# Kernel optimization log

Hardware: AMD Instinct MI355X
Metric: run time of the kernel (lower is better)

The kernel has to match this reference:

```python
import jax, jax.numpy as jnp
import numpy as np

DIM = 256
HEADS = 8
CAMS = 6
MINSIZE = 25  # AdaptiveAvgPool2d output size = min(feature_map_size)


def layernorm(x, g, b, eps=1e-5):
    mu = x.mean(-1, keepdims=True)
    var = ((x - mu) ** 2).mean(-1, keepdims=True)
    return (x - mu) / jnp.sqrt(var + eps) * g + b


def setup_inputs() -> dict:
    key = jax.random.key(0)
    ks = jax.random.split(key, 16)
    d, n = DIM, CAMS
    s = 0.02
    inp = {}
    inp["q"] = jax.random.normal(ks[0], (2, n, d, 50, 50), jnp.float32)
    inp["k"] = jax.random.normal(ks[1], (2, n, d, 50, 50), jnp.float32)
    inp["v"] = jax.random.normal(ks[2], (2, n, d, 50, 50), jnp.float32)
    inp["Wq"] = jax.random.normal(ks[3], (d, d), jnp.float32) * s
    inp["bq"] = jnp.zeros((d,), jnp.float32)
    inp["Wk"] = jax.random.normal(ks[4], (d, d), jnp.float32) * s
    inp["bk"] = jnp.zeros((d,), jnp.float32)
    inp["Wv"] = jax.random.normal(ks[5], (d, d), jnp.float32) * s
    inp["bv"] = jnp.zeros((d,), jnp.float32)
    inp["Wproj"] = jax.random.normal(ks[6], (n * d, d), jnp.float32) * s
    inp["bproj"] = jnp.zeros((d,), jnp.float32)
    inp["Waddq"] = jax.random.normal(ks[7], (n * d, d), jnp.float32) * s
    inp["baddq"] = jnp.zeros((d,), jnp.float32)
    inp["W1"] = jax.random.normal(ks[8], (d, 2 * d), jnp.float32) * s
    inp["b1"] = jnp.zeros((2 * d,), jnp.float32)
    inp["W2"] = jax.random.normal(ks[9], (2 * d, d), jnp.float32) * s
    inp["b2"] = jnp.zeros((d,), jnp.float32)
    inp["g_pre"] = jnp.ones((n * d,), jnp.float32)
    inp["b_pre"] = jnp.zeros((n * d,), jnp.float32)
    inp["g_norm"] = jnp.ones((d,), jnp.float32)
    inp["b_norm"] = jnp.zeros((d,), jnp.float32)
    return inp


def reference(q, k, v, Wq, bq, Wk, bk, Wv, bv, Wproj, bproj, Waddq, baddq,
              W1, b1, W2, b2, g_pre, b_pre, g_norm, b_norm):
    B, n, d, H, W = q.shape
    m = HEADS
    dh = d // m
    Q = H * W

    # residual query path: (b n d H W) -> (b HW (n d)) -> add_qproj -> (b HW d)
    add_q = jnp.transpose(q, (0, 3, 4, 1, 2)).reshape(B, Q, n * d) @ Waddq + baddq

    # queries: (b n d H W) -> (b n HW d) -> to_q
    qf = jnp.transpose(q, (0, 1, 3, 4, 2)).reshape(B, n, Q, d) @ Wq + bq

    # adaptive avg pool to MINSIZE (exact 2x2 bins since 50 = 2*25)
    def pool(t):
        _, _, _, h, w = t.shape
        return t.reshape(B, n, d, MINSIZE, h // MINSIZE, MINSIZE, w // MINSIZE).mean((4, 6))

    kp = pool(k)  # (b n d 25 25)
    vp = pool(v)
    K = MINSIZE * MINSIZE
    # (avg pool commutes with the pointwise linear to_k/to_v)
    kf = jnp.transpose(kp, (0, 1, 3, 4, 2)).reshape(B, n, K, d) @ Wk + bk
    vf = jnp.transpose(vp, (0, 1, 3, 4, 2)).reshape(B, n, K, d) @ Wv + bv

    # split heads
    qh = qf.reshape(B, n, Q, m, dh)
    kh = kf.reshape(B, n, K, m, dh)
    vh = vf.reshape(B, n, K, m, dh)

    # per-camera scores, softmax jointly over concatenated camera keys
    scores = (dh ** -0.5) * jnp.einsum('bnqmd,bnkmd->bmqnk', qh, kh)  # (B,m,Q,n,K)
    attn = jax.nn.softmax(scores.reshape(B, m, Q, n * K), axis=-1).reshape(B, m, Q, n, K)

    # per-camera attention output, concat cams (and heads within each cam) -> (B,Q,n*d)
    out = jnp.einsum('bmqnk,bnkmd->bqnmd', attn, vh).reshape(B, Q, n * d)

    x = layernorm(out, g_pre, b_pre) @ Wproj + bproj  # (B,Q,d)
    x = x + add_q
    h1 = jax.nn.gelu(x @ W1 + b1, approximate=False)
    x = x + layernorm(h1 @ W2 + b2, g_norm, b_norm)
    return jnp.transpose(x.reshape(B, H, W, d), (0, 3, 1, 2))  # (B,d,H,W)
```

## Files before the change

kernel.cpp:

```cpp
#include <hip/hip_runtime.h>
#include <math.h>

#define BATCH 2
#define NCAM 6
#define DIM 256
#define HEADS 8
#define DH 32
#define HW 2500
#define KP 625
#define NDIM (NCAM*DIM)

typedef __attribute__((ext_vector_type(8))) short short8;
typedef __attribute__((ext_vector_type(4))) float f32x4;

__device__ __forceinline__ short f2bf(float f) {
    union { float f; unsigned u; } v; v.f = f;
    unsigned r = v.u + 0x7fffu + ((v.u >> 16) & 1u);
    return (short)(r >> 16);
}
__device__ __forceinline__ float bf2f(short h) {
    union { unsigned u; float f; } v; v.u = ((unsigned)(unsigned short)h) << 16;
    return v.f;
}

struct WJ { const float* src; short* dst; int K, N; };
struct WArgs { WJ j[7]; };

__global__ __launch_bounds__(256) void prep_all(
    const float* __restrict__ q, const float* __restrict__ k,
    const float* __restrict__ v, short* __restrict__ qbf,
    short* __restrict__ kpbf, short* __restrict__ vpbf, WArgs wa)
{
    __shared__ float t[32][33];
    const int tx = threadIdx.x & 31, ty = threadIdx.x >> 5;
    int i = blockIdx.x;
    if (i < 7584) {
        int slab = i / 632, rem = i % 632;
        int hwB = (rem % 79) * 32, dB = (rem / 79) * 32;
        const float* src = q + (size_t)slab * 640000;
#pragma unroll
        for (int ii = 0; ii < 32; ii += 8) {
            int hw = hwB + tx;
            t[ty + ii][tx] = (hw < HW) ? src[(size_t)(dB + ty + ii) * HW + hw] : 0.f;
        }
        __syncthreads();
#pragma unroll
        for (int ii = 0; ii < 32; ii += 8) {
            int hw = hwB + ty + ii;
            if (hw < HW)
                qbf[((size_t)slab * HW + hw) * DIM + dB + tx] = f2bf(t[tx][ty + ii]);
        }
    } else if (i < 11424) {
        int i2 = i - 7584;
        const float* base; short* dst;
        if (i2 < 1920) { base = k; dst = kpbf; }
        else           { base = v; dst = vpbf; i2 -= 1920; }
        int slab = i2 / 160, rem = i2 % 160;
        int kpB = (rem % 20) * 32, dB = (rem / 20) * 32;
        const float* src = base + (size_t)slab * 640000;
        dst += (size_t)slab * (KP * DIM);
#pragma unroll
        for (int ii = 0; ii < 32; ii += 8) {
            int kp = kpB + tx;
            float val = 0.f;
            if (kp < KP) {
                int r2 = (kp / 25) * 2, c2 = (kp % 25) * 2;
                const float* p0 = src + (size_t)(dB + ty + ii) * HW + r2 * 50 + c2;
                val = 0.25f * (p0[0] + p0[1] + p0[50] + p0[51]);
            }
            t[ty + ii][tx] = val;
        }
        __syncthreads();
#pragma unroll
        for (int ii = 0; ii < 32; ii += 8) {
            int kp = kpB + ty + ii;
            if (kp < KP)
                dst[(size_t)kp * DIM + dB + tx] = f2bf(t[tx][ty + ii]);
        }
    } else {
        int wi = i - 11424;
        WJ jb = wa.j[0];
        for (int jj = 0; jj < 7; jj++) {
            jb = wa.j[jj];
            int cnt = (jb.K >> 5) * (jb.N >> 5);
            if (wi < cnt) break;
            wi -= cnt;
        }
        int tn = jb.N >> 5;
        int nB = (wi % tn) * 32, kB = (wi / tn) * 32;
#pragma unroll
        for (int ii = 0; ii < 32; ii += 8)
            t[ty + ii][tx] = jb.src[(size_t)(kB + ty + ii) * jb.N + nB + tx];
        __syncthreads();
#pragma unroll
        for (int ii = 0; ii < 32; ii += 8)
            jb.dst[(size_t)(nB + ty + ii) * jb.K + kB + tx] = f2bf(t[tx][ty + ii]);
    }
}

struct GJob { const short* A; const short* Bt; const float* bias;
              short* Cb; float* Cf; int M, K, yb, mode; };
struct GArgs { GJob j[4]; };

__global__ __launch_bounds__(256) void gemm_in(GArgs ga) {
    GJob jb = ga.j[blockIdx.z];
    if ((int)blockIdx.y >= jb.yb) return;
    __shared__ short As[128 * 32];
    __shared__ short Bs[64 * 32];

    const int tid  = threadIdx.x;
    const int nB   = blockIdx.x * 64;
    const int rB   = blockIdx.y * 128;
    const int w    = tid >> 6;
    const int lane = tid & 63;
    const int l15  = lane & 15;
    const int quad = lane >> 4;
    const int M = jb.M, K = jb.K;

    f32x4 acc[2][4];
#pragma unroll
    for (int i = 0; i < 2; i++)
#pragma unroll
        for (int jt = 0; jt < 4; jt++) acc[i][jt] = (f32x4){0.f, 0.f, 0.f, 0.f};

    const int ra = tid >> 1, k0 = (tid & 1) * 16;
    const int rga = rB + ra;
    const int bb = rga / 2500, hwp = rga % 2500;
    const int nb_ = tid >> 2, gkb = tid & 3;

    short8 pa0 = {0,0,0,0,0,0,0,0}, pa1 = pa0, pb = pa0;
    if (rga < M) {
        if (jb.mode) {
            int cam = k0 >> 8, c = k0 & 255;
            const short* p = &jb.A[(((size_t)(bb * 6 + cam)) * HW + hwp) * DIM + c];
            pa0 = *(const short8*)p; pa1 = *(const short8*)(p + 8);
        } else {
            const short* p = &jb.A[(size_t)rga * K + k0];
            pa0 = *(const short8*)p; pa1 = *(const short8*)(p + 8);
        }
    }
    pb = *(const short8*)&jb.Bt[(size_t)(nB + nb_) * K + gkb * 8];

    for (int kB = 0; kB < K; kB += 32) {
        __syncthreads();
        {
            int g0 = k0 >> 3;
            *(short8*)&As[ra * 32 + ((g0 ^ (ra & 3)) << 3)]       = pa0;
            *(short8*)&As[ra * 32 + (((g0 + 1) ^ (ra & 3)) << 3)] = pa1;
            *(short8*)&Bs[nb_ * 32 + ((gkb ^ (nb_ & 3)) << 3)]    = pb;
        }
        __syncthreads();
        int kN = kB + 32;
        if (kN < K) {
            if (rga < M) {
                if (jb.mode) {
                    int kk = kN + k0;
                    int cam = kk >> 8, c = kk & 255;
                    const short* p = &jb.A[(((size_t)(bb * 6 + cam)) * HW + hwp) * DIM + c];
                    pa0 = *(const short8*)p; pa1 = *(const short8*)(p + 8);
                } else {
                    const short* p = &jb.A[(size_t)rga * K + kN + k0];
                    pa0 = *(const short8*)p; pa1 = *(const short8*)(p + 8);
                }
            }
            pb = *(const short8*)&jb.Bt[(size_t)(nB + nb_) * K + kN + gkb * 8];
        }
        short8 af[2], bfr[4];
#pragma unroll
        for (int i = 0; i < 2; i++) {
            int m = w * 32 + i * 16 + l15;
            af[i] = *(const short8*)&As[m * 32 + ((quad ^ (m & 3)) << 3)];
        }
#pragma unroll
        for (int jt = 0; jt < 4; jt++) {
            int n = jt * 16 + l15;
            bfr[jt] = *(const short8*)&Bs[n * 32 + ((quad ^ (n & 3)) << 3)];
        }
#pragma unroll
        for (int i = 0; i < 2; i++)
#pragma unroll
            for (int jt = 0; jt < 4; jt++)
                acc[i][jt] = __builtin_amdgcn_mfma_f32_16x16x32_bf16(
                    af[i], bfr[jt], acc[i][jt], 0, 0, 0);
    }
#pragma unroll
    for (int i = 0; i < 2; i++) {
        int rbase = rB + w * 32 + i * 16 + quad * 4;
#pragma unroll
        for (int jt = 0; jt < 4; jt++) {
            int col = nB + jt * 16 + l15;
            float bcol = jb.bias[col];
#pragma unroll
            for (int reg = 0; reg < 4; reg++) {
                int rr = rbase + reg;
                if (rr < M) {
                    float vv = acc[i][jt][reg] + bcol;
                    if (jb.Cb) jb.Cb[(size_t)rr * 256 + col] = f2bf(vv);
                    else       jb.Cf[(size_t)rr * 256 + col] = vv;
                }
            }
        }
    }
}

template<int EPI, int WF32, int WBF>
__global__ __launch_bounds__(256) void mgemm_bf(
    const short* __restrict__ A, const short* __restrict__ Bt,
    const float* __restrict__ bias, const float* __restrict__ res,
    float* __restrict__ C, short* __restrict__ C2, int M, int N, int K)
{
    __shared__ short As[128 * 32];
    __shared__ short Bs[64 * 32];

    const int tid  = threadIdx.x;
    const int nB   = blockIdx.x * 64;
    const int rB   = blockIdx.y * 128;
    const int w    = tid >> 6;
    const int lane = tid & 63;
    const int l15  = lane & 15;
    const int quad = lane >> 4;

    f32x4 acc[2][4];
#pragma unroll
    for (int i = 0; i < 2; i++)
#pragma unroll
        for (int jt = 0; jt < 4; jt++) acc[i][jt] = (f32x4){0.f, 0.f, 0.f, 0.f};

    const int ra = tid >> 1, k0 = (tid & 1) * 16;
    const int rga = rB + ra;
    const int nb_ = tid >> 2, gkb = tid & 3;

    short8 pa0 = {0,0,0,0,0,0,0,0}, pa1 = pa0, pb = pa0;
    if (rga < M) {
        const short* p = &A[(size_t)rga * K + k0];
        pa0 = *(const short8*)p; pa1 = *(const short8*)(p + 8);
    }
    pb = *(const short8*)&Bt[(size_t)(nB + nb_) * K + gkb * 8];

    for (int kB = 0; kB < K; kB += 32) {
        __syncthreads();
        {
            int g0 = k0 >> 3;
            *(short8*)&As[ra * 32 + ((g0 ^ (ra & 3)) << 3)]       = pa0;
            *(short8*)&As[ra * 32 + (((g0 + 1) ^ (ra & 3)) << 3)] = pa1;
            *(short8*)&Bs[nb_ * 32 + ((gkb ^ (nb_ & 3)) << 3)]    = pb;
        }
        __syncthreads();
        int kN = kB + 32;
        if (kN < K) {
            if (rga < M) {
                const short* p = &A[(size_t)rga * K + kN + k0];
                pa0 = *(const short8*)p; pa1 = *(const short8*)(p + 8);
            }
            pb = *(const short8*)&Bt[(size_t)(nB + nb_) * K + kN + gkb * 8];
        }
        short8 af[2], bfr[4];
#pragma unroll
        for (int i = 0; i < 2; i++) {
            int m = w * 32 + i * 16 + l15;
            af[i] = *(const short8*)&As[m * 32 + ((quad ^ (m & 3)) << 3)];
        }
#pragma unroll
        for (int jt = 0; jt < 4; jt++) {
            int n = jt * 16 + l15;
            bfr[jt] = *(const short8*)&Bs[n * 32 + ((quad ^ (n & 3)) << 3)];
        }
#pragma unroll
        for (int i = 0; i < 2; i++)
#pragma unroll
            for (int jt = 0; jt < 4; jt++)
                acc[i][jt] = __builtin_amdgcn_mfma_f32_16x16x32_bf16(
                    af[i], bfr[jt], acc[i][jt], 0, 0, 0);
    }
#pragma unroll
    for (int i = 0; i < 2; i++) {
        int rbase = rB + w * 32 + i * 16 + quad * 4;
#pragma unroll
        for (int jt = 0; jt < 4; jt++) {
            int col = nB + jt * 16 + l15;
            float bcol = bias[col];
#pragma unroll
            for (int reg = 0; reg < 4; reg++) {
                int rr = rbase + reg;
                if (rr < M) {
                    float vv = acc[i][jt][reg] + bcol;
                    if (EPI == 1) vv = 0.5f * vv * (1.f + erff(vv * 0.70710678118654752f));
                    if (EPI == 2) vv += res[(size_t)rr * N + col];
                    if (WF32) C[(size_t)rr * N + col] = vv;
                    if (WBF)  C2[(size_t)rr * N + col] = f2bf(vv);
                }
            }
        }
    }
}

#define TQA 64
#define CH 64
#define VSTR 72

__global__ __launch_bounds__(256) void attn_mfma(
    const short* __restrict__ qf, const short* __restrict__ kf,
    const short* __restrict__ vf, short* __restrict__ attn_out,
    float* __restrict__ Zp)
{
    const int qt  = blockIdx.x;
    const int bm  = blockIdx.y;
    const int cam = blockIdx.z;
    const int b = bm >> 3, m = bm & 7;
    const int q0 = qt * TQA;
    const int tid = threadIdx.x;
    const int w = tid >> 6, lane = tid & 63;
    const int l15 = lane & 15, quad = lane >> 4;

    __shared__ __align__(16) short Ks[CH][DH];
    __shared__ __align__(16) short Vt[DH][VSTR];
    __shared__ __align__(16) short Pl[TQA][VSTR];

    const size_t slab = (size_t)(b * 6 + cam);

    int qrow = q0 + w * 16 + l15;
    int qcl  = qrow < HW ? qrow : HW - 1;
    const short8 aq = *(const short8*)&qf[(slab * HW + qcl) * DIM + m * DH + quad * 8];

    const short* kb = kf + slab * KP * DIM + m * DH;
    const short* vb = vf + slab * KP * DIM + m * DH;

    f32x4 oacc[2];
    oacc[0] = (f32x4){0.f, 0.f, 0.f, 0.f};
    oacc[1] = (f32x4){0.f, 0.f, 0.f, 0.f};
    float zp[4] = {0.f, 0.f, 0.f, 0.f};
    const float scale = 0.17677669529663687f;

    const int kl = tid >> 2, d8 = (tid & 3) * 8;
    const int vcol = (((kl >> 3) ^ (d8 >> 3)) << 3) | (kl & 7);

    for (int c0 = 0; c0 < KP; c0 += CH) {
        __syncthreads();
        {
            int key = c0 + kl;
            short8 kv8 = {0, 0, 0, 0, 0, 0, 0, 0};
            short8 vv8 = {0, 0, 0, 0, 0, 0, 0, 0};
            if (key < KP) {
                kv8 = *(const short8*)&kb[(size_t)key * DIM + d8];
                vv8 = *(const short8*)&vb[(size_t)key * DIM + d8];
            }
            *(short8*)&Ks[kl][d8] = kv8;
#pragma unroll
            for (int t = 0; t < 8; t++) Vt[d8 + t][vcol] = vv8[t];
        }
        __syncthreads();
        f32x4 sfrag[4];
#pragma unroll
        for (int jt = 0; jt < 4; jt++) {
            short8 bk8 = *(const short8*)&Ks[jt * 16 + l15][quad * 8];
            sfrag[jt] = __builtin_amdgcn_mfma_f32_16x16x32_bf16(
                aq, bk8, (f32x4){0.f, 0.f, 0.f, 0.f}, 0, 0, 0);
        }
#pragma unroll
        for (int jt = 0; jt < 4; jt++) {
            bool valid = (c0 + jt * 16 + l15) < KP;
#pragma unroll
            for (int reg = 0; reg < 4; reg++) {
                float p = valid ? __expf(scale * sfrag[jt][reg]) : 0.f;
                short ph = f2bf(p);
                zp[reg] += bf2f(ph);
                Pl[w * 16 + quad * 4 + reg][jt * 16 + l15] = ph;
            }
        }
#pragma unroll
        for (int ks = 0; ks < 2; ks++) {
            short8 ap = *(const short8*)&Pl[w * 16 + l15][ks * 32 + quad * 8];
#pragma unroll
            for (int nt = 0; nt < 2; nt++) {
                int dhn = nt * 16 + l15;
                int pgrp = ((ks * 4 + quad) ^ (dhn >> 3));
                short8 bv8 = *(const short8*)&Vt[dhn][pgrp << 3];
                oacc[nt] = __builtin_amdgcn_mfma_f32_16x16x32_bf16(
                    ap, bv8, oacc[nt], 0, 0, 0);
            }
        }
    }
#pragma unroll
    for (int off = 1; off < 16; off <<= 1)
#pragma unroll
        for (int reg = 0; reg < 4; reg++)
            zp[reg] += __shfl_xor(zp[reg], off, 64);
#pragma unroll
    for (int reg = 0; reg < 4; reg++) {
        int q = q0 + w * 16 + quad * 4 + reg;
        if (q < HW) {
            size_t rowb = ((size_t)b * HW + q) * NDIM + cam * DIM + m * DH;
            attn_out[rowb + l15]      = f2bf(oacc[0][reg]);
            attn_out[rowb + 16 + l15] = f2bf(oacc[1][reg]);
            if (l15 == 0)
                Zp[((size_t)bm * 6 + cam) * HW + q] = zp[reg];
        }
    }
}

__global__ __launch_bounds__(256) void ln_pre_kernel(
    const short* __restrict__ xin, short* __restrict__ lnbf,
    const float* __restrict__ Zp,
    const float* __restrict__ g, const float* __restrict__ bt)
{
    const int row = blockIdx.x;
    const int tid = threadIdx.x;
    const int b = row / 2500, q = row % 2500;
    __shared__ float zinv[8];
    if (tid < 8) {
        float z = 0.f;
#pragma unroll
        for (int cam = 0; cam < 6; cam++)
            z += Zp[((size_t)(b * 8 + tid) * 6 + cam) * HW + q];
        zinv[tid] = 1.f / z;
    }
    __syncthreads();
    const short* p = xin + (size_t)row * NDIM;
    float v[6];
    float s = 0.f, ss = 0.f;
#pragma unroll
    for (int i = 0; i < 6; i++) {
        int c = tid + i * 256;
        v[i] = bf2f(p[c]) * zinv[(c >> 5) & 7];
        s += v[i]; ss += v[i] * v[i];
    }
    __shared__ float rs[4], rss[4];
    int lane = tid & 63, wid = tid >> 6;
#pragma unroll
    for (int o = 32; o > 0; o >>= 1) { s += __shfl_down(s, o); ss += __shfl_down(ss, o); }
    if (lane == 0) { rs[wid] = s; rss[wid] = ss; }
    __syncthreads();
    s = rs[0] + rs[1] + rs[2] + rs[3];
    ss = rss[0] + rss[1] + rss[2] + rss[3];
    float mu = s * (1.f / NDIM);
    float var = ss * (1.f / NDIM) - mu * mu;
    float inv = rsqrtf(var + 1e-5f);
#pragma unroll
    for (int i = 0; i < 6; i++) {
        int c = tid + i * 256;
        lnbf[(size_t)row * NDIM + c] = f2bf((v[i] - mu) * inv * g[c] + bt[c]);
    }
}

__global__ __launch_bounds__(256) void final_kernel2(
    const float* __restrict__ x, const float* __restrict__ y2,
    const float* __restrict__ g, const float* __restrict__ bt,
    float* __restrict__ out)
{
    __shared__ float T[256][33];
    __shared__ float ps[32][8], pss[32][8];
    __shared__ float mu_s[32], inv_s[32];
    const int tid = threadIdx.x;
    const int rl = tid & 31, seg = tid >> 5;
    const int r0 = blockIdx.x * 32;
    const int row = r0 + rl;
    const bool ok = row < 5000;

    float4 yv[8];
    float s = 0.f, ss = 0.f;
    if (ok) {
        const float4* yp = (const float4*)(y2 + (size_t)row * DIM + seg * 32);
#pragma unroll
        for (int j = 0; j < 8; j++) {
            yv[j] = yp[j];
            s += yv[j].x + yv[j].y + yv[j].z + yv[j].w;
            ss += yv[j].x * yv[j].x + yv[j].y * yv[j].y
                + yv[j].z * yv[j].z + yv[j].w * yv[j].w;
        }
    } else {
#pragma unroll
        for (int j = 0; j < 8; j++) yv[j] = (float4){0, 0, 0, 0};
    }
    ps[rl][seg] = s; pss[rl][seg] = ss;
    __syncthreads();
    if (tid < 32) {
        float a = 0.f, b2 = 0.f;
#pragma unroll
        for (int j = 0; j < 8; j++) { a += ps[tid][j]; b2 += pss[tid][j]; }
        float mu = a * (1.f / DIM);
        float var = b2 * (1.f / DIM) - mu * mu;
        mu_s[tid] = mu;
        inv_s[tid] = rsqrtf(var + 1e-5f);
    }
    __syncthreads();
    if (ok) {
        float mu = mu_s[rl], inv = inv_s[rl];
        const float4* xp = (const float4*)(x + (size_t)row * DIM + seg * 32);
#pragma unroll
        for (int j = 0; j < 8; j++) {
            float4 xv = xp[j];
            int c = seg * 32 + j * 4;
            T[c + 0][rl] = xv.x + (yv[j].x - mu) * inv * g[c + 0] + bt[c + 0];
            T[c + 1][rl] = xv.y + (yv[j].y - mu) * inv * g[c + 1] + bt[c + 1];
            T[c + 2][rl] = xv.z + (yv[j].z - mu) * inv * g[c + 2] + bt[c + 2];
            T[c + 3][rl] = xv.w + (yv[j].w - mu) * inv * g[c + 3] + bt[c + 3];
        }
    }
    __syncthreads();
    const int w = tid >> 6, lane = tid & 63;
    const int hl = lane & 31, ch = lane >> 5;
    const int rr = r0 + hl;
    if (rr < 5000) {
        int b = rr / 2500, hw = rr % 2500;
        size_t obase = (size_t)b * 640000 + hw;
#pragma unroll
        for (int it = 0; it < 32; it++) {
            int c = it * 8 + w * 2 + ch;
            out[obase + (size_t)c * 2500] = T[c][hl];
        }
    }
}

extern "C" void kernel_launch(void* const* d_in, const int* in_sizes, int n_in,
                              void* d_out, int out_size, void* d_ws, size_t ws_size,
                              hipStream_t stream)
{
    const float* q     = (const float*)d_in[0];
    const float* k     = (const float*)d_in[1];
    const float* v     = (const float*)d_in[2];
    const float* Wq    = (const float*)d_in[3];
    const float* bq    = (const float*)d_in[4];
    const float* Wk    = (const float*)d_in[5];
    const float* bk    = (const float*)d_in[6];
    const float* Wv    = (const float*)d_in[7];
    const float* bv    = (const float*)d_in[8];
    const float* Wproj = (const float*)d_in[9];
    const float* bproj = (const float*)d_in[10];
    const float* Waddq = (const float*)d_in[11];
    const float* baddq = (const float*)d_in[12];
    const float* W1    = (const float*)d_in[13];
    const float* b1    = (const float*)d_in[14];
    const float* W2    = (const float*)d_in[15];
    const float* b2    = (const float*)d_in[16];
    const float* g_pre = (const float*)d_in[17];
    const float* b_pre = (const float*)d_in[18];
    const float* g_nrm = (const float*)d_in[19];
    const float* b_nrm = (const float*)d_in[20];
    float* out = (float*)d_out;

    float* ws = (float*)d_ws;
    short* qf_a   = (short*)(ws);
    short* lnbf   = (short*)(ws);
    short* qbf    = (short*)(ws + 3840000);
    short* kf_a   = (short*)(ws + 7680000);
    short* kpbf   = (short*)(ws + 8640000);
    short* vf_a   = (short*)(ws + 9600000);
    short* vpbf   = (short*)(ws + 10560000);
    float* add_q  = ws + 11520000;
    short* attn_o = (short*)(ws + 12800000);
    short* xbf    = (short*)(ws + 12800000);
    short* h1bf   = (short*)(ws + 13440000);
    float* x      = ws + 20480000;
    float* Zp     = ws + 21760000;
    short* eW     = (short*)(ws + 22000000);
    short* Wq_t    = eW;
    short* Wk_t    = eW + 65536;
    short* Wv_t    = eW + 131072;
    short* Waddq_t = eW + 196608;
    short* lW     = (short*)(ws + 22295000);
    short* Wproj_t = lW;
    short* W1_t    = lW + 393216;
    short* W2_t    = lW + 524288;
    float* y2     = ws + 22625000;

    dim3 blk(256);

    {
        WArgs wa;
        wa.j[0] = {Wq,    Wq_t,    256,  256};
        wa.j[1] = {Wk,    Wk_t,    256,  256};
        wa.j[2] = {Wv,    Wv_t,    256,  256};
        wa.j[3] = {Waddq, Waddq_t, 1536, 256};
        wa.j[4] = {Wproj, Wproj_t, 1536, 256};
        wa.j[5] = {W1,    W1_t,    256,  512};
        wa.j[6] = {W2,    W2_t,    512,  256};
        prep_all<<<dim3(12640), blk, 0, stream>>>(q, k, v, qbf, kpbf, vpbf, wa);
    }
    {
        GArgs ga;
        ga.j[0] = {qbf,  Wq_t,    bq,    qf_a, nullptr, 30000, 256,  235, 0};
        ga.j[1] = {kpbf, Wk_t,    bk,    kf_a, nullptr, 7500,  256,  59,  0};
        ga.j[2] = {vpbf, Wv_t,    bv,    vf_a, nullptr, 7500,  256,  59,  0};
        ga.j[3] = {qbf,  Waddq_t, baddq, nullptr, add_q, 5000, 1536, 40,  1};
        gemm_in<<<dim3(4, 235, 4), blk, 0, stream>>>(ga);
    }
    attn_mfma<<<dim3(40, 16, 6), blk, 0, stream>>>(qf_a, kf_a, vf_a, attn_o, Zp);
    ln_pre_kernel<<<dim3(5000), blk, 0, stream>>>(attn_o, lnbf, Zp, g_pre, b_pre);
    mgemm_bf<2, 1, 1><<<dim3(4, 40), blk, 0, stream>>>(
        lnbf, Wproj_t, bproj, add_q, x, xbf, 5000, 256, 1536);
    mgemm_bf<1, 0, 1><<<dim3(8, 40), blk, 0, stream>>>(
        xbf, W1_t, b1, nullptr, nullptr, h1bf, 5000, 512, 256);
    mgemm_bf<0, 1, 0><<<dim3(4, 40), blk, 0, stream>>>(
        h1bf, W2_t, b2, nullptr, y2, nullptr, 5000, 256, 512);
    final_kernel2<<<dim3(157), blk, 0, stream>>>(x, y2, g_nrm, b_nrm, out);
}
```

Before: 342.6 us.

## Transpose score MFMA and pack P/V shared-memory stores in attention kernel

Swaps the MFMA operands so each lane holds four consecutive keys for one query row. The exp results can then be packed with v_cvt_pk_bf16_f32 into a single 64-bit LDS store, replacing per-element scattered stores. The row-sum reduction drops from a 4-step shuffle to 2 steps. V staging now loads pairs of keys and writes packed 32-bit words into the transposed V tile instead of eight 16-bit stores, and the full chunks skip bounds checks. Z is now accumulated from fp32 exp values rather than bf16-rounded ones, a slight numerical change.

```diff
diff --git a/kernel.cpp b/kernel.cpp
--- a/kernel.cpp
+++ b/kernel.cpp
@@ -11,6 +11,7 @@
 #define NDIM (NCAM*DIM)
 
 typedef __attribute__((ext_vector_type(8))) short short8;
+typedef __attribute__((ext_vector_type(4))) short short4s;
 typedef __attribute__((ext_vector_type(4))) float f32x4;
 
 __device__ __forceinline__ short f2bf(float f) {
@@ -328,43 +329,70 @@
     f32x4 oacc[2];
     oacc[0] = (f32x4){0.f, 0.f, 0.f, 0.f};
     oacc[1] = (f32x4){0.f, 0.f, 0.f, 0.f};
-    float zp[4] = {0.f, 0.f, 0.f, 0.f};
+    float zp = 0.f;
     const float scale = 0.17677669529663687f;
 
     const int kl = tid >> 2, d8 = (tid & 3) * 8;
-    const int vcol = (((kl >> 3) ^ (d8 >> 3)) << 3) | (kl & 7);
+    const int kp2 = tid >> 3, dv = (tid & 7) * 4;
+    const int vcol2 = (((kp2 >> 2) ^ (dv >> 3)) << 3) | ((2 * kp2) & 7);
 
     for (int c0 = 0; c0 < KP; c0 += CH) {
         __syncthreads();
         {
             int key = c0 + kl;
             short8 kv8 = {0, 0, 0, 0, 0, 0, 0, 0};
-            short8 vv8 = {0, 0, 0, 0, 0, 0, 0, 0};
-            if (key < KP) {
-                kv8 = *(const short8*)&kb[(size_t)key * DIM + d8];
-                vv8 = *(const short8*)&vb[(size_t)key * DIM + d8];
-            }
+            if (key < KP) kv8 = *(const short8*)&kb[(size_t)key * DIM + d8];
             *(short8*)&Ks[kl][d8] = kv8;
-#pragma unroll
-            for (int t = 0; t < 8; t++) Vt[d8 + t][vcol] = vv8[t];
-        }
-        __syncthreads();
-        f32x4 sfrag[4];
+
+            int k0v = c0 + 2 * kp2;
+            short4s v0 = {0, 0, 0, 0}, v1 = {0, 0, 0, 0};
+            if (k0v < KP)     v0 = *(const short4s*)&vb[(size_t)k0v * DIM + dv];
+            if (k0v + 1 < KP) v1 = *(const short4s*)&vb[(size_t)(k0v + 1) * DIM + dv];
+#pragma unroll
+            for (int t = 0; t < 4; t++) {
+                unsigned pk = (unsigned)(unsigned short)v0[t]
+                            | ((unsigned)(unsigned short)v1[t] << 16);
+                *(unsigned*)&Vt[dv + t][vcol2] = pk;
+            }
+        }
+        __syncthreads();
+        f32x4 sfragT[4];
 #pragma unroll
         for (int jt = 0; jt < 4; jt++) {
             short8 bk8 = *(const short8*)&Ks[jt * 16 + l15][quad * 8];
-            sfrag[jt] = __builtin_amdgcn_mfma_f32_16x16x32_bf16(
-                aq, bk8, (f32x4){0.f, 0.f, 0.f, 0.f}, 0, 0, 0);
-        }
-#pragma unroll
-        for (int jt = 0; jt < 4; jt++) {
-            bool valid = (c0 + jt * 16 + l15) < KP;
-#pragma unroll
-            for (int reg = 0; reg < 4; reg++) {
-                float p = valid ? __expf(scale * sfrag[jt][reg]) : 0.f;
-                short ph = f2bf(p);
-                zp[reg] += bf2f(ph);
-                Pl[w * 16 + quad * 4 + reg][jt * 16 + l15] = ph;
+            sfragT[jt] = __builtin_amdgcn_mfma_f32_16x16x32_bf16(
+                bk8, aq, (f32x4){0.f, 0.f, 0.f, 0.f}, 0, 0, 0);
+        }
+        short* prow = &Pl[w * 16 + l15][0];
+        if (c0 + CH <= KP) {
+#pragma unroll
+            for (int jt = 0; jt < 4; jt++) {
+                float e0 = __expf(scale * sfragT[jt][0]);
+                float e1 = __expf(scale * sfragT[jt][1]);
+                float e2 = __expf(scale * sfragT[jt][2]);
+                float e3 = __expf(scale * sfragT[jt][3]);
+                zp += (e0 + e1) + (e2 + e3);
+                unsigned lo, hi;
+                asm("v_cvt_pk_bf16_f32 %0, %1, %2" : "=v"(lo) : "v"(e0), "v"(e1));
+                asm("v_cvt_pk_bf16_f32 %0, %1, %2" : "=v"(hi) : "v"(e2), "v"(e3));
+                unsigned long long pk64 = ((unsigned long long)hi << 32) | (unsigned long long)lo;
+                *(unsigned long long*)&prow[jt * 16 + quad * 4] = pk64;
+            }
+        } else {
+            int kbase = c0 + quad * 4;
+#pragma unroll
+            for (int jt = 0; jt < 4; jt++) {
+                int kb0 = kbase + jt * 16;
+                float e0 = (kb0 + 0 < KP) ? __expf(scale * sfragT[jt][0]) : 0.f;
+                float e1 = (kb0 + 1 < KP) ? __expf(scale * sfragT[jt][1]) : 0.f;
+                float e2 = (kb0 + 2 < KP) ? __expf(scale * sfragT[jt][2]) : 0.f;
+                float e3 = (kb0 + 3 < KP) ? __expf(scale * sfragT[jt][3]) : 0.f;
+                zp += (e0 + e1) + (e2 + e3);
+                unsigned lo, hi;
+                asm("v_cvt_pk_bf16_f32 %0, %1, %2" : "=v"(lo) : "v"(e0), "v"(e1));
+                asm("v_cvt_pk_bf16_f32 %0, %1, %2" : "=v"(hi) : "v"(e2), "v"(e3));
+                unsigned long long pk64 = ((unsigned long long)hi << 32) | (unsigned long long)lo;
+                *(unsigned long long*)&prow[jt * 16 + quad * 4] = pk64;
             }
         }
 #pragma unroll
@@ -380,11 +408,12 @@
             }
         }
     }
-#pragma unroll
-    for (int off = 1; off < 16; off <<= 1)
-#pragma unroll
-        for (int reg = 0; reg < 4; reg++)
-            zp[reg] += __shfl_xor(zp[reg], off, 64);
+    zp += __shfl_xor(zp, 16, 64);
+    zp += __shfl_xor(zp, 32, 64);
+    if (quad == 0) {
+        int q = q0 + w * 16 + l15;
+        if (q < HW) Zp[((size_t)bm * 6 + cam) * HW + q] = zp;
+    }
 #pragma unroll
     for (int reg = 0; reg < 4; reg++) {
         int q = q0 + w * 16 + quad * 4 + reg;
@@ -392,8 +421,6 @@
             size_t rowb = ((size_t)b * HW + q) * NDIM + cam * DIM + m * DH;
             attn_out[rowb + l15]      = f2bf(oacc[0][reg]);
             attn_out[rowb + 16 + l15] = f2bf(oacc[1][reg]);
-            if (l15 == 0)
-                Zp[((size_t)bm * 6 + cam) * HW + q] = zp[reg];
         }
     }
 }
```

Result: faster. 331.8 us (-3.2%).
